# Optimization experiments

Measured on AMD Instinct MI355X. Metric: run time of the kernel, lower is better.

The kernel has to match this reference:

```python
import jax, jax.numpy as jnp
import numpy as np

B, N, CT = 64, 256, 3
HID, HEADS = 256, 4
C = HID // HEADS          # per-head channels
E = 8192                  # number of edges
NEG = 0.2                 # GATv2 leaky_relu negative slope
EPS_BN = 1e-5


def setup_inputs() -> dict:
    key = jax.random.key(0)
    ks = jax.random.split(key, 32)
    F_in = N * CT
    s1 = 1.0 / np.sqrt(F_in)
    sh = 1.0 / np.sqrt(HID)
    inp = {
        "x": jax.random.normal(ks[0], (B, N, N, CT), jnp.float32),
        "edge_index": jax.random.randint(ks[1], (2, E), 0, N, dtype=jnp.int32),
        # node_proj: Linear + BatchNorm1d (eval) params
        "W1": jax.random.normal(ks[2], (F_in, HID), jnp.float32) * s1,
        "b1": jnp.zeros((HID,), jnp.float32),
        "g1": jnp.ones((HID,), jnp.float32),
        "be1": jnp.zeros((HID,), jnp.float32),
        "m1": jnp.zeros((HID,), jnp.float32),
        "v1": jnp.ones((HID,), jnp.float32),
        # GATv2 layer 0
        "Wl0": jax.random.normal(ks[3], (HID, HID), jnp.float32) * sh,
        "bl0": jnp.zeros((HID,), jnp.float32),
        "Wr0": jax.random.normal(ks[4], (HID, HID), jnp.float32) * sh,
        "br0": jnp.zeros((HID,), jnp.float32),
        "att0": jax.random.normal(ks[5], (HEADS, C), jnp.float32) * (1.0 / np.sqrt(C)),
        "bo0": jnp.zeros((HID,), jnp.float32),
        # GATv2 layer 1
        "Wl1": jax.random.normal(ks[6], (HID, HID), jnp.float32) * sh,
        "bl1": jnp.zeros((HID,), jnp.float32),
        "Wr1": jax.random.normal(ks[7], (HID, HID), jnp.float32) * sh,
        "br1": jnp.zeros((HID,), jnp.float32),
        "att1": jax.random.normal(ks[8], (HEADS, C), jnp.float32) * (1.0 / np.sqrt(C)),
        "bo1": jnp.zeros((HID,), jnp.float32),
        # output_proj: Linear + BatchNorm1d (eval) params
        "W2": jax.random.normal(ks[9], (HID, HID), jnp.float32) * sh,
        "b2": jnp.zeros((HID,), jnp.float32),
        "g2": jnp.ones((HID,), jnp.float32),
        "be2": jnp.zeros((HID,), jnp.float32),
        "m2": jnp.zeros((HID,), jnp.float32),
        "v2": jnp.ones((HID,), jnp.float32),
    }
    return inp


def _bn(x, g, b, m, v):
    # BatchNorm1d in eval mode: per-feature affine with running stats
    return (x - m) * jax.lax.rsqrt(v + EPS_BN) * g + b


def _gatv2(h, src, dst, Wl, bl, Wr, br, att, bo):
    # h: (N, HID). GATv2Conv (PyG semantics): lin_l on source, lin_r on target.
    xl = (h @ Wl + bl).reshape(N, HEADS, C)
    xr = (h @ Wr + br).reshape(N, HEADS, C)
    x_j = xl[src]                        # (E, H, C) source features
    x_i = xr[dst]                        # (E, H, C) target features
    e = jax.nn.leaky_relu(x_i + x_j, NEG)
    logits = jnp.einsum('ehc,hc->eh', e, att)          # (E, H)
    mx = jax.ops.segment_max(logits, dst, num_segments=N)
    a = jnp.exp(logits - mx[dst])
    den = jax.ops.segment_sum(a, dst, num_segments=N)
    a = a / (den[dst] + 1e-16)                         # neighborhood softmax
    out = jax.ops.segment_sum(x_j * a[:, :, None], dst, num_segments=N)
    return out.reshape(N, HID) + bo


def reference(x, edge_index, W1, b1, g1, be1, m1, v1,
              Wl0, bl0, Wr0, br0, att0, bo0,
              Wl1, bl1, Wr1, br1, att1, bo1,
              W2, b2, g2, be2, m2, v2):
    gelu = lambda t: jax.nn.gelu(t, approximate=False)
    xf = x.reshape(B, N, N * CT)
    # node_proj (eval: dropout off, BN uses running stats -> vmappable)
    h = gelu(_bn(xf @ W1 + b1, g1, be1, m1, v1))       # (B, N, HID)
    src, dst = edge_index[0], edge_index[1]

    def per_sample(hn):
        h0 = gelu(_gatv2(hn, src, dst, Wl0, bl0, Wr0, br0, att0, bo0))
        h1 = gelu(_gatv2(h0, src, dst, Wl1, bl1, Wr1, br1, att1, bo1))
        return h1.mean(axis=0)                          # mean over nodes

    pooled = jax.vmap(per_sample)(h)                    # (B, HID)
    return gelu(_bn(pooled @ W2 + b2, g2, be2, m2, v2))
```

## Files before the change

### kernel.cpp

```cpp
#include <hip/hip_runtime.h>
#include <hip/hip_bf16.h>
#include <math.h>

#define BATCH   64
#define NNODES  256
#define HID     256
#define HEADS   4
#define CDIM    64
#define NEDGES  8192
#define NEG_SLOPE 0.2f
#define EPS_BN 1e-5f


typedef __bf16 bf16_t;
typedef __bf16 bf16x8 __attribute__((ext_vector_type(8)));
typedef float  f32x4  __attribute__((ext_vector_type(4)));

__device__ __forceinline__ float gelu_f(float x) {
    return 0.5f * x * (1.0f + erff(x * 0.70710678118654752440f));
}

__global__ __launch_bounds__(256) void csr_kernel(const int* __restrict__ ei,
                                                  int* __restrict__ noff,
                                                  int* __restrict__ csrc) {
    __shared__ int cnt[NNODES];
    __shared__ int off_s[NNODES + 1];
    const int tid = threadIdx.x;
    cnt[tid] = 0;
    __syncthreads();
    for (int e = tid; e < NEDGES; e += 256) atomicAdd(&cnt[ei[NEDGES + e]], 1);
    __syncthreads();
    if (tid == 0) {
        int s = 0;
        for (int i = 0; i < NNODES; ++i) { off_s[i] = s; s += cnt[i]; }
        off_s[NNODES] = s;
    }
    __syncthreads();
    cnt[tid] = off_s[tid];
    noff[tid] = off_s[tid];
    if (tid == 0) noff[NNODES] = off_s[NNODES];
    __syncthreads();
    for (int e = tid; e < NEDGES; e += 256) {
        int d = ei[NEDGES + e];
        int p = atomicAdd(&cnt[d], 1);
        csrc[p] = ei[e];
    }
}

__global__ __launch_bounds__(256) void trans_kernel(
        const float* __restrict__ W1, const float* __restrict__ Wa,
        const float* __restrict__ Wb, const float* __restrict__ Wc,
        const float* __restrict__ Wd,
        bf16_t* __restrict__ T1, bf16_t* __restrict__ Ta,
        bf16_t* __restrict__ Tb, bf16_t* __restrict__ Tc,
        bf16_t* __restrict__ Td) {
    __shared__ float tile[32][33];
    int bx = blockIdx.x;
    const float* in; bf16_t* out; int K, t;
    if (bx < 192) { in = W1; out = T1; K = 768; t = bx; }
    else {
        int r = bx - 192, mid = r >> 6; t = r & 63; K = 256;
        if (mid == 0) { in = Wa; out = Ta; }
        else if (mid == 1) { in = Wb; out = Tb; }
        else if (mid == 2) { in = Wc; out = Tc; }
        else { in = Wd; out = Td; }
    }
    const int kt = t >> 3, nt = t & 7;
    const int k0 = kt * 32, n0 = nt * 32;
    const int x = threadIdx.x, y = threadIdx.y;
    #pragma unroll
    for (int j = 0; j < 4; ++j)
        tile[y + j * 8][x] = in[(size_t)(k0 + y + j * 8) * 256 + n0 + x];
    __syncthreads();
    #pragma unroll
    for (int j = 0; j < 4; ++j)
        out[(size_t)(n0 + y + j * 8) * K + k0 + x] = (bf16_t)tile[x][y + j * 8];
}

#define GSTR 56

template<int A_F32, int DUAL, int EPI_BN, int PERM>
__global__ __launch_bounds__(256) void gemm_kernel(
        const void* __restrict__ Ap,
        const bf16_t* __restrict__ Bt0, const bf16_t* __restrict__ Bt1,
        void* __restrict__ C0p, void* __restrict__ C1p, int K,
        const float* __restrict__ bias0, const float* __restrict__ bias1,
        const float* __restrict__ g, const float* __restrict__ be,
        const float* __restrict__ mu, const float* __restrict__ var) {
    __shared__ bf16_t As[128][GSTR];
    __shared__ bf16_t Bs[64][GSTR];
    const int tid  = threadIdx.x;
    const int lane = tid & 63;
    const int wv   = tid >> 6;
    const int wm   = wv >> 1, wn = wv & 1;
    const int mblk = blockIdx.y * 128;
    const int nt   = blockIdx.x;
    const bool second = DUAL && (nt >= 4);
    const bf16_t* Bt = second ? Bt1 : Bt0;
    const int n0 = (second ? (nt - 4) : nt) * 64;

    f32x4 acc[8];
    #pragma unroll
    for (int i = 0; i < 8; ++i) acc[i] = (f32x4){0.f, 0.f, 0.f, 0.f};

    const int arow = tid >> 1, akh = (tid & 1) * 16;
    const int gr   = mblk + arow;
    const int arr  = PERM ? ((gr & 63) * 256 + (gr >> 6)) : gr;
    const int brow = tid >> 2, bkh = (tid & 3) * 8;
    const int fm = lane & 15, kc = (lane >> 4) * 8;

    for (int k0 = 0; k0 < K; k0 += 32) {
        if (A_F32) {
            const float* ap = (const float*)Ap + (size_t)arr * K + k0 + akh;
            f32x4 a0 = *(const f32x4*)ap;
            f32x4 a1 = *(const f32x4*)(ap + 4);
            f32x4 a2 = *(const f32x4*)(ap + 8);
            f32x4 a3 = *(const f32x4*)(ap + 12);
            bf16x8 v0, v1;
            #pragma unroll
            for (int j = 0; j < 4; ++j) {
                v0[j] = (bf16_t)a0[j]; v0[4 + j] = (bf16_t)a1[j];
                v1[j] = (bf16_t)a2[j]; v1[4 + j] = (bf16_t)a3[j];
            }
            *(bf16x8*)(&As[arow][akh])     = v0;
            *(bf16x8*)(&As[arow][akh + 8]) = v1;
        } else {
            const bf16_t* ap = (const bf16_t*)Ap + (size_t)arr * K + k0 + akh;
            *(bf16x8*)(&As[arow][akh])     = *(const bf16x8*)ap;
            *(bf16x8*)(&As[arow][akh + 8]) = *(const bf16x8*)(ap + 8);
        }
        *(bf16x8*)(&Bs[brow][bkh]) =
            *(const bf16x8*)(Bt + (size_t)(n0 + brow) * K + k0 + bkh);
        __syncthreads();

        bf16x8 af[4], bf[2];
        #pragma unroll
        for (int f = 0; f < 4; ++f)
            af[f] = *(const bf16x8*)(&As[wm * 64 + f * 16 + fm][kc]);
        #pragma unroll
        for (int t = 0; t < 2; ++t)
            bf[t] = *(const bf16x8*)(&Bs[wn * 32 + t * 16 + fm][kc]);
        #pragma unroll
        for (int f = 0; f < 4; ++f)
            #pragma unroll
            for (int t = 0; t < 2; ++t)
                acc[f * 2 + t] = __builtin_amdgcn_mfma_f32_16x16x32_bf16(
                    af[f], bf[t], acc[f * 2 + t], 0, 0, 0);
        __syncthreads();
    }

    const int quad = lane >> 4, cn = lane & 15;
    #pragma unroll
    for (int t = 0; t < 2; ++t) {
        const int n = n0 + wn * 32 + t * 16 + cn;
        const float bv = second ? bias1[n] : bias0[n];
        float scale = 1.0f, shift = 0.0f;
        if (EPI_BN) {
            float s = g[n] * rsqrtf(var[n] + EPS_BN);
            scale = s;
            shift = be[n] - mu[n] * s;
        }
        #pragma unroll
        for (int f = 0; f < 4; ++f) {
            #pragma unroll
            for (int r = 0; r < 4; ++r) {
                const int m = mblk + wm * 64 + f * 16 + quad * 4 + r;
                float val = acc[f * 2 + t][r] + bv;
                if (EPI_BN) val = gelu_f(val * scale + shift);
                if (second) ((float*)C1p)[(size_t)m * 256 + n] = val;
                else        ((bf16_t*)C0p)[(size_t)m * 256 + n] = (bf16_t)val;
            }
        }
    }
}

template<int OUT_F32>
__global__ __launch_bounds__(256) void edge_kernel(
        const bf16_t* __restrict__ XL, const float* __restrict__ XR,
        const float* __restrict__ att, const float* __restrict__ bo,
        const int* __restrict__ noff, const int* __restrict__ csrc,
        void* __restrict__ Hout) {
    const int i    = blockIdx.x;
    const int tid  = threadIdx.x;
    const int w    = tid >> 6;
    const int lane = tid & 63;
    const int bg   = lane >> 3;
    const int cg   = lane & 7;
    const int b    = blockIdx.y * 8 + bg;
    const int cbase = w * CDIM + cg * 8;
    const size_t orow = ((size_t)i * BATCH + b) * HID + cbase;

    float a6[8], a4[8], xi[8];
    {
        const float* ar = att + cbase;
        const float* xr = XR + orow;
        #pragma unroll
        for (int q = 0; q < 8; ++q) {
            float a = ar[q];
            a6[q] = 0.6f * a; a4[q] = 0.4f * a;
            xi[q] = xr[q];
        }
    }
    const int s0 = noff[i], s1 = noff[i + 1];

    float m = -1e30f, den = 0.f;
    float acc[8];
    #pragma unroll
    for (int q = 0; q < 8; ++q) acc[q] = 0.f;

    const bf16_t* XLb = XL + (size_t)b * HID + cbase;

    int jc = csrc[s0 < s1 ? s0 : 0];
    bf16x8 xjp = *(const bf16x8*)(XLb + (size_t)jc * (BATCH * HID));

    for (int e = s0; e < s1; ++e) {
        const int en = e + 1;
        const int jn = csrc[en < s1 ? en : s0];
        const bf16x8 xjn = *(const bf16x8*)(XLb + (size_t)jn * (BATCH * HID));

        float xjf[8];
        #pragma unroll
        for (int q = 0; q < 8; ++q) xjf[q] = (float)xjp[q];
        float p = 0.f;
        #pragma unroll
        for (int q = 0; q < 8; ++q) {
            const float z = xi[q] + xjf[q];
            p = fmaf(a6[q], z, p);
            p = fmaf(a4[q], __builtin_fabsf(z), p);
        }
        p += __shfl_xor(p, 1, 64);
        p += __shfl_xor(p, 2, 64);
        p += __shfl_xor(p, 4, 64);

        const float mn = fmaxf(m, p);
        const float alpha = __expf(m - mn);
        const float we = __expf(p - mn);
        den = den * alpha + we;
        #pragma unroll
        for (int q = 0; q < 8; ++q) acc[q] = fmaf(acc[q], alpha, we * xjf[q]);
        m = mn;
        xjp = xjn;
    }

    const float inv = 1.0f / (den + 1e-16f);
    const float* bor = bo + cbase;
    if (OUT_F32) {
        float* op = (float*)Hout + orow;
        #pragma unroll
        for (int q = 0; q < 8; ++q)
            op[q] = gelu_f(acc[q] * inv + bor[q]);
    } else {
        bf16x8 ov;
        #pragma unroll
        for (int q = 0; q < 8; ++q)
            ov[q] = (bf16_t)gelu_f(acc[q] * inv + bor[q]);
        *(bf16x8*)((bf16_t*)Hout + orow) = ov;
    }
}

__global__ __launch_bounds__(256) void pool_kernel(const float* __restrict__ H1,
                                                   float* __restrict__ P) {
    const int b = blockIdx.x, c = blockIdx.y, f = threadIdx.x;
    float s = 0.f;
    for (int n = 0; n < 64; ++n)
        s += H1[((size_t)(c * 64 + n) * BATCH + b) * HID + f];
    P[((size_t)b * 4 + c) * HID + f] = s;
}

__global__ __launch_bounds__(256) void final_kernel(
        const float* __restrict__ P, const float* __restrict__ W2,
        const float* __restrict__ b2, const float* __restrict__ g2,
        const float* __restrict__ be2, const float* __restrict__ m2,
        const float* __restrict__ v2, float* __restrict__ out) {
    __shared__ float pl[HID];
    const int b = blockIdx.x, f = threadIdx.x;
    float s4 = 0.f;
    #pragma unroll
    for (int c = 0; c < 4; ++c) s4 += P[((size_t)b * 4 + c) * HID + f];
    pl[f] = s4 * (1.0f / (float)NNODES);
    __syncthreads();
    float s = 0.f;
    for (int k = 0; k < HID; ++k) s += pl[k] * W2[(size_t)k * HID + f];
    s += b2[f];
    const float scale = g2[f] * rsqrtf(v2[f] + EPS_BN);
    s = (s - m2[f]) * scale + be2[f];
    out[b * HID + f] = gelu_f(s);
}

extern "C" void kernel_launch(void* const* d_in, const int* in_sizes, int n_in,
                              void* d_out, int out_size, void* d_ws, size_t ws_size,
                              hipStream_t stream) {
    const float* x    = (const float*)d_in[0];
    const int*   ei   = (const int*)d_in[1];
    const float* W1   = (const float*)d_in[2];
    const float* b1   = (const float*)d_in[3];
    const float* g1   = (const float*)d_in[4];
    const float* be1  = (const float*)d_in[5];
    const float* m1   = (const float*)d_in[6];
    const float* v1   = (const float*)d_in[7];
    const float* Wl0  = (const float*)d_in[8];
    const float* bl0  = (const float*)d_in[9];
    const float* Wr0  = (const float*)d_in[10];
    const float* br0  = (const float*)d_in[11];
    const float* att0 = (const float*)d_in[12];
    const float* bo0  = (const float*)d_in[13];
    const float* Wl1  = (const float*)d_in[14];
    const float* bl1  = (const float*)d_in[15];
    const float* Wr1  = (const float*)d_in[16];
    const float* br1  = (const float*)d_in[17];
    const float* att1 = (const float*)d_in[18];
    const float* bo1  = (const float*)d_in[19];
    const float* W2   = (const float*)d_in[20];
    const float* b2   = (const float*)d_in[21];
    const float* g2   = (const float*)d_in[22];
    const float* be2  = (const float*)d_in[23];
    const float* m2   = (const float*)d_in[24];
    const float* v2   = (const float*)d_in[25];

    char* ws = (char*)d_ws;
    const int M = BATCH * NNODES;
    const size_t SZ_BF = (size_t)M * HID * sizeof(bf16_t);
    const size_t SZ_F  = (size_t)M * HID * sizeof(float);

    int*    noff = (int*)ws;                ws += 2048;
    int*    csrc = (int*)ws;                ws += 32768;
    bf16_t* W1t  = (bf16_t*)ws;             ws += 256 * 768 * 2;
    bf16_t* Wl0t = (bf16_t*)ws;             ws += 256 * 256 * 2;
    bf16_t* Wr0t = (bf16_t*)ws;             ws += 256 * 256 * 2;
    bf16_t* Wl1t = (bf16_t*)ws;             ws += 256 * 256 * 2;
    bf16_t* Wr1t = (bf16_t*)ws;             ws += 256 * 256 * 2;
    bf16_t* H    = (bf16_t*)ws;             ws += SZ_BF;
    bf16_t* H2   = (bf16_t*)ws;             ws += SZ_BF;
    bf16_t* XL   = (bf16_t*)ws;             ws += SZ_BF;
    float*  XR   = (float*)ws;              ws += SZ_F;
    float*  H1f  = (float*)ws;              ws += SZ_F;
    float*  P    = (float*)ws;              ws += BATCH * 4 * HID * 4;

    csr_kernel<<<1, 256, 0, stream>>>(ei, noff, csrc);
    trans_kernel<<<448, dim3(32, 8), 0, stream>>>(W1, Wl0, Wr0, Wl1, Wr1,
                                                  W1t, Wl0t, Wr0t, Wl1t, Wr1t);

    gemm_kernel<1, 0, 1, 1><<<dim3(4, 128), 256, 0, stream>>>(
        x, W1t, nullptr, H, nullptr, 768, b1, nullptr, g1, be1, m1, v1);

    gemm_kernel<0, 1, 0, 0><<<dim3(8, 128), 256, 0, stream>>>(
        H, Wl0t, Wr0t, XL, XR, 256, bl0, br0, nullptr, nullptr, nullptr, nullptr);
    edge_kernel<0><<<dim3(NNODES, 8), 256, 0, stream>>>(
        XL, XR, att0, bo0, noff, csrc, H2);

    gemm_kernel<0, 1, 0, 0><<<dim3(8, 128), 256, 0, stream>>>(
        H2, Wl1t, Wr1t, XL, XR, 256, bl1, br1, nullptr, nullptr, nullptr, nullptr);
    edge_kernel<1><<<dim3(NNODES, 8), 256, 0, stream>>>(
        XL, XR, att1, bo1, noff, csrc, H1f);

    pool_kernel<<<dim3(BATCH, 4), 256, 0, stream>>>(H1f, P);
    final_kernel<<<BATCH, 256, 0, stream>>>(P, W2, b2, g2, be2, m2, v2,
                                            (float*)d_out);
}
```

Measured before the change: 318.4 us.

## Merge prep kernels, store XR and layer outputs in bf16, dual-chain edge softmax

Merges the CSR build and weight transposes into one launch, and stores the right-projection XR and the final GAT output in bf16 instead of fp32 to cut memory traffic. The edge kernel now runs two independent online-softmax chains over alternating edges for more ILP, merges them at the end, and short-circuits nodes with no incoming edges. The pool and final kernels are fused into one kernel that reads bf16 H directly. The trade-offs are reduced precision in XR and the final activations, and a serial 256-node loop per thread in the fused pool kernel.

```diff
diff --git a/kernel.cpp b/kernel.cpp
--- a/kernel.cpp
+++ b/kernel.cpp
@@ -20,42 +20,42 @@
     return 0.5f * x * (1.0f + erff(x * 0.70710678118654752440f));
 }
 
-__global__ __launch_bounds__(256) void csr_kernel(const int* __restrict__ ei,
-                                                  int* __restrict__ noff,
-                                                  int* __restrict__ csrc) {
-    __shared__ int cnt[NNODES];
-    __shared__ int off_s[NNODES + 1];
-    const int tid = threadIdx.x;
-    cnt[tid] = 0;
-    __syncthreads();
-    for (int e = tid; e < NEDGES; e += 256) atomicAdd(&cnt[ei[NEDGES + e]], 1);
-    __syncthreads();
-    if (tid == 0) {
-        int s = 0;
-        for (int i = 0; i < NNODES; ++i) { off_s[i] = s; s += cnt[i]; }
-        off_s[NNODES] = s;
-    }
-    __syncthreads();
-    cnt[tid] = off_s[tid];
-    noff[tid] = off_s[tid];
-    if (tid == 0) noff[NNODES] = off_s[NNODES];
-    __syncthreads();
-    for (int e = tid; e < NEDGES; e += 256) {
-        int d = ei[NEDGES + e];
-        int p = atomicAdd(&cnt[d], 1);
-        csrc[p] = ei[e];
-    }
-}
-
-__global__ __launch_bounds__(256) void trans_kernel(
+__global__ __launch_bounds__(256) void prep_kernel(
+        const int* __restrict__ ei,
         const float* __restrict__ W1, const float* __restrict__ Wa,
         const float* __restrict__ Wb, const float* __restrict__ Wc,
         const float* __restrict__ Wd,
+        int* __restrict__ noff, int* __restrict__ csrc,
         bf16_t* __restrict__ T1, bf16_t* __restrict__ Ta,
         bf16_t* __restrict__ Tb, bf16_t* __restrict__ Tc,
         bf16_t* __restrict__ Td) {
+    const int bx = blockIdx.x;
+    const int tid = threadIdx.x;
+    if (bx == 448) {
+        __shared__ int cnt[NNODES];
+        __shared__ int off_s[NNODES + 1];
+        cnt[tid] = 0;
+        __syncthreads();
+        for (int e = tid; e < NEDGES; e += 256) atomicAdd(&cnt[ei[NEDGES + e]], 1);
+        __syncthreads();
+        if (tid == 0) {
+            int s = 0;
+            for (int i = 0; i < NNODES; ++i) { off_s[i] = s; s += cnt[i]; }
+            off_s[NNODES] = s;
+        }
+        __syncthreads();
+        cnt[tid] = off_s[tid];
+        noff[tid] = off_s[tid];
+        if (tid == 0) noff[NNODES] = off_s[NNODES];
+        __syncthreads();
+        for (int e = tid; e < NEDGES; e += 256) {
+            int d = ei[NEDGES + e];
+            int p = atomicAdd(&cnt[d], 1);
+            csrc[p] = ei[e];
+        }
+        return;
+    }
     __shared__ float tile[32][33];
-    int bx = blockIdx.x;
     const float* in; bf16_t* out; int K, t;
     if (bx < 192) { in = W1; out = T1; K = 768; t = bx; }
     else {
@@ -67,7 +67,7 @@
     }
     const int kt = t >> 3, nt = t & 7;
     const int k0 = kt * 32, n0 = nt * 32;
-    const int x = threadIdx.x, y = threadIdx.y;
+    const int x = tid & 31, y = tid >> 5;
     #pragma unroll
     for (int j = 0; j < 4; ++j)
         tile[y + j * 8][x] = in[(size_t)(k0 + y + j * 8) * 256 + n0 + x];
@@ -83,7 +83,7 @@
 __global__ __launch_bounds__(256) void gemm_kernel(
         const void* __restrict__ Ap,
         const bf16_t* __restrict__ Bt0, const bf16_t* __restrict__ Bt1,
-        void* __restrict__ C0p, void* __restrict__ C1p, int K,
+        bf16_t* __restrict__ C0p, bf16_t* __restrict__ C1p, int K,
         const float* __restrict__ bias0, const float* __restrict__ bias1,
         const float* __restrict__ g, const float* __restrict__ be,
         const float* __restrict__ mu, const float* __restrict__ var) {
@@ -97,6 +97,7 @@
     const int nt   = blockIdx.x;
     const bool second = DUAL && (nt >= 4);
     const bf16_t* Bt = second ? Bt1 : Bt0;
+    bf16_t* Cp = second ? C1p : C0p;
     const int n0 = (second ? (nt - 4) : nt) * 64;
 
     f32x4 acc[8];
@@ -167,124 +168,136 @@
                 const int m = mblk + wm * 64 + f * 16 + quad * 4 + r;
                 float val = acc[f * 2 + t][r] + bv;
                 if (EPI_BN) val = gelu_f(val * scale + shift);
-                if (second) ((float*)C1p)[(size_t)m * 256 + n] = val;
-                else        ((bf16_t*)C0p)[(size_t)m * 256 + n] = (bf16_t)val;
+                Cp[(size_t)m * 256 + n] = (bf16_t)val;
             }
         }
     }
 }
 
-template<int OUT_F32>
 __global__ __launch_bounds__(256) void edge_kernel(
-        const bf16_t* __restrict__ XL, const float* __restrict__ XR,
+        const bf16_t* __restrict__ XL, const bf16_t* __restrict__ XR,
         const float* __restrict__ att, const float* __restrict__ bo,
         const int* __restrict__ noff, const int* __restrict__ csrc,
-        void* __restrict__ Hout) {
-    const int i    = blockIdx.x;
+        bf16_t* __restrict__ Hout) {
+    const int bid  = blockIdx.x;
+    const int i    = bid >> 3;
     const int tid  = threadIdx.x;
     const int w    = tid >> 6;
     const int lane = tid & 63;
     const int bg   = lane >> 3;
     const int cg   = lane & 7;
-    const int b    = blockIdx.y * 8 + bg;
+    const int b    = (bid & 7) * 8 + bg;
     const int cbase = w * CDIM + cg * 8;
     const size_t orow = ((size_t)i * BATCH + b) * HID + cbase;
+    const float* bor = bo + cbase;
+
+    const int s0 = noff[i], s1 = noff[i + 1];
+    if (s0 == s1) {
+        bf16x8 ov;
+        #pragma unroll
+        for (int q = 0; q < 8; ++q) ov[q] = (bf16_t)gelu_f(bor[q]);
+        *(bf16x8*)(Hout + orow) = ov;
+        return;
+    }
 
     float a6[8], a4[8], xi[8];
     {
         const float* ar = att + cbase;
-        const float* xr = XR + orow;
+        const bf16x8 xr = *(const bf16x8*)(XR + orow);
         #pragma unroll
         for (int q = 0; q < 8; ++q) {
             float a = ar[q];
             a6[q] = 0.6f * a; a4[q] = 0.4f * a;
-            xi[q] = xr[q];
-        }
-    }
-    const int s0 = noff[i], s1 = noff[i + 1];
-
-    float m = -1e30f, den = 0.f;
-    float acc[8];
-    #pragma unroll
-    for (int q = 0; q < 8; ++q) acc[q] = 0.f;
+            xi[q] = (float)xr[q];
+        }
+    }
 
     const bf16_t* XLb = XL + (size_t)b * HID + cbase;
-
-    int jc = csrc[s0 < s1 ? s0 : 0];
-    bf16x8 xjp = *(const bf16x8*)(XLb + (size_t)jc * (BATCH * HID));
-
-    for (int e = s0; e < s1; ++e) {
-        const int en = e + 1;
-        const int jn = csrc[en < s1 ? en : s0];
-        const bf16x8 xjn = *(const bf16x8*)(XLb + (size_t)jn * (BATCH * HID));
-
-        float xjf[8];
-        #pragma unroll
-        for (int q = 0; q < 8; ++q) xjf[q] = (float)xjp[q];
-        float p = 0.f;
+    const size_t RSTR = (size_t)BATCH * HID;
+
+    float mA = -1e30f, dA = 0.f, mB = -1e30f, dB = 0.f;
+    float accA[8], accB[8];
+    #pragma unroll
+    for (int q = 0; q < 8; ++q) { accA[q] = 0.f; accB[q] = 0.f; }
+
+    int jA = csrc[s0];
+    int jB = csrc[(s0 + 1 < s1) ? s0 + 1 : s0];
+    bf16x8 xA = *(const bf16x8*)(XLb + (size_t)jA * RSTR);
+    bf16x8 xB = *(const bf16x8*)(XLb + (size_t)jB * RSTR);
+
+    for (int e = s0; e < s1; e += 2) {
+        const int nA = (e + 2 < s1) ? e + 2 : s0;
+        const int nB = (e + 3 < s1) ? e + 3 : s0;
+        const int jnA = csrc[nA], jnB = csrc[nB];
+        const bf16x8 xnA = *(const bf16x8*)(XLb + (size_t)jnA * RSTR);
+        const bf16x8 xnB = *(const bf16x8*)(XLb + (size_t)jnB * RSTR);
+
+        float fA[8], fB[8];
+        #pragma unroll
+        for (int q = 0; q < 8; ++q) { fA[q] = (float)xA[q]; fB[q] = (float)xB[q]; }
+        float pA = 0.f, pB = 0.f;
         #pragma unroll
         for (int q = 0; q < 8; ++q) {
-            const float z = xi[q] + xjf[q];
-            p = fmaf(a6[q], z, p);
-            p = fmaf(a4[q], __builtin_fabsf(z), p);
-        }
-        p += __shfl_xor(p, 1, 64);
-        p += __shfl_xor(p, 2, 64);
-        p += __shfl_xor(p, 4, 64);
-
-        const float mn = fmaxf(m, p);
-        const float alpha = __expf(m - mn);
-        const float we = __expf(p - mn);
-        den = den * alpha + we;
-        #pragma unroll
-        for (int q = 0; q < 8; ++q) acc[q] = fmaf(acc[q], alpha, we * xjf[q]);
-        m = mn;
-        xjp = xjn;
-    }
-
-    const float inv = 1.0f / (den + 1e-16f);
-    const float* bor = bo + cbase;
-    if (OUT_F32) {
-        float* op = (float*)Hout + orow;
-        #pragma unroll
-        for (int q = 0; q < 8; ++q)
-            op[q] = gelu_f(acc[q] * inv + bor[q]);
-    } else {
-        bf16x8 ov;
-        #pragma unroll
-        for (int q = 0; q < 8; ++q)
-            ov[q] = (bf16_t)gelu_f(acc[q] * inv + bor[q]);
-        *(bf16x8*)((bf16_t*)Hout + orow) = ov;
-    }
-}
-
-__global__ __launch_bounds__(256) void pool_kernel(const float* __restrict__ H1,
-                                                   float* __restrict__ P) {
-    const int b = blockIdx.x, c = blockIdx.y, f = threadIdx.x;
-    float s = 0.f;
-    for (int n = 0; n < 64; ++n)
-        s += H1[((size_t)(c * 64 + n) * BATCH + b) * HID + f];
-    P[((size_t)b * 4 + c) * HID + f] = s;
-}
-
-__global__ __launch_bounds__(256) void final_kernel(
-        const float* __restrict__ P, const float* __restrict__ W2,
+            const float zA = xi[q] + fA[q];
+            const float zB = xi[q] + fB[q];
+            pA = fmaf(a6[q], zA, pA);
+            pB = fmaf(a6[q], zB, pB);
+            pA = fmaf(a4[q], __builtin_fabsf(zA), pA);
+            pB = fmaf(a4[q], __builtin_fabsf(zB), pB);
+        }
+        pA += __shfl_xor(pA, 1, 64);  pB += __shfl_xor(pB, 1, 64);
+        pA += __shfl_xor(pA, 2, 64);  pB += __shfl_xor(pB, 2, 64);
+        pA += __shfl_xor(pA, 4, 64);  pB += __shfl_xor(pB, 4, 64);
+
+        const float mnA = fmaxf(mA, pA);
+        const float alA = __expf(mA - mnA);
+        const float wA  = __expf(pA - mnA);
+        const float vB  = (e + 1 < s1) ? 1.f : 0.f;
+        const float mnB = fmaxf(mB, pB);
+        const float alB = __expf(mB - mnB);
+        const float wB  = __expf(pB - mnB) * vB;
+        dA = dA * alA + wA;
+        dB = dB * alB + wB;
+        #pragma unroll
+        for (int q = 0; q < 8; ++q) {
+            accA[q] = fmaf(accA[q], alA, wA * fA[q]);
+            accB[q] = fmaf(accB[q], alB, wB * fB[q]);
+        }
+        mA = mnA; mB = mnB;
+        xA = xnA; xB = xnB;
+    }
+
+    const float mm = fmaxf(mA, mB);
+    const float g1 = __expf(mA - mm);
+    const float g2 = __expf(mB - mm);
+    const float inv = 1.0f / (dA * g1 + dB * g2 + 1e-16f);
+    bf16x8 ov;
+    #pragma unroll
+    for (int q = 0; q < 8; ++q) {
+        const float o = (accA[q] * g1 + accB[q] * g2) * inv + bor[q];
+        ov[q] = (bf16_t)gelu_f(o);
+    }
+    *(bf16x8*)(Hout + orow) = ov;
+}
+
+__global__ __launch_bounds__(256) void pf_kernel(
+        const bf16_t* __restrict__ H1, const float* __restrict__ W2,
         const float* __restrict__ b2, const float* __restrict__ g2,
         const float* __restrict__ be2, const float* __restrict__ m2,
         const float* __restrict__ v2, float* __restrict__ out) {
     __shared__ float pl[HID];
     const int b = blockIdx.x, f = threadIdx.x;
-    float s4 = 0.f;
-    #pragma unroll
-    for (int c = 0; c < 4; ++c) s4 += P[((size_t)b * 4 + c) * HID + f];
-    pl[f] = s4 * (1.0f / (float)NNODES);
+    float s = 0.f;
+    for (int n = 0; n < NNODES; ++n)
+        s += (float)H1[((size_t)n * BATCH + b) * HID + f];
+    pl[f] = s * (1.0f / (float)NNODES);
     __syncthreads();
-    float s = 0.f;
-    for (int k = 0; k < HID; ++k) s += pl[k] * W2[(size_t)k * HID + f];
-    s += b2[f];
+    float acc = 0.f;
+    for (int k = 0; k < HID; ++k) acc += pl[k] * W2[(size_t)k * HID + f];
+    acc += b2[f];
     const float scale = g2[f] * rsqrtf(v2[f] + EPS_BN);
-    s = (s - m2[f]) * scale + be2[f];
-    out[b * HID + f] = gelu_f(s);
+    acc = (acc - m2[f]) * scale + be2[f];
+    out[b * HID + f] = gelu_f(acc);
 }
 
 extern "C" void kernel_launch(void* const* d_in, const int* in_sizes, int n_in,
@@ -320,7 +333,6 @@
     char* ws = (char*)d_ws;
     const int M = BATCH * NNODES;
     const size_t SZ_BF = (size_t)M * HID * sizeof(bf16_t);
-    const size_t SZ_F  = (size_t)M * HID * sizeof(float);
 
     int*    noff = (int*)ws;                ws += 2048;
     int*    csrc = (int*)ws;                ws += 32768;
@@ -332,28 +344,21 @@
     bf16_t* H    = (bf16_t*)ws;             ws += SZ_BF;
     bf16_t* H2   = (bf16_t*)ws;             ws += SZ_BF;
     bf16_t* XL   = (bf16_t*)ws;             ws += SZ_BF;
-    float*  XR   = (float*)ws;              ws += SZ_F;
-    float*  H1f  = (float*)ws;              ws += SZ_F;
-    float*  P    = (float*)ws;              ws += BATCH * 4 * HID * 4;
-
-    csr_kernel<<<1, 256, 0, stream>>>(ei, noff, csrc);
-    trans_kernel<<<448, dim3(32, 8), 0, stream>>>(W1, Wl0, Wr0, Wl1, Wr1,
-                                                  W1t, Wl0t, Wr0t, Wl1t, Wr1t);
+    bf16_t* XR   = (bf16_t*)ws;             ws += SZ_BF;
+
+    prep_kernel<<<449, 256, 0, stream>>>(ei, W1, Wl0, Wr0, Wl1, Wr1,
+                                         noff, csrc, W1t, Wl0t, Wr0t, Wl1t, Wr1t);
 
     gemm_kernel<1, 0, 1, 1><<<dim3(4, 128), 256, 0, stream>>>(
         x, W1t, nullptr, H, nullptr, 768, b1, nullptr, g1, be1, m1, v1);
 
     gemm_kernel<0, 1, 0, 0><<<dim3(8, 128), 256, 0, stream>>>(
         H, Wl0t, Wr0t, XL, XR, 256, bl0, br0, nullptr, nullptr, nullptr, nullptr);
-    edge_kernel<0><<<dim3(NNODES, 8), 256, 0, stream>>>(
-        XL, XR, att0, bo0, noff, csrc, H2);
+    edge_kernel<<<NNODES * 8, 256, 0, stream>>>(XL, XR, att0, bo0, noff, csrc, H2);
 
     gemm_kernel<0, 1, 0, 0><<<dim3(8, 128), 256, 0, stream>>>(
         H2, Wl1t, Wr1t, XL, XR, 256, bl1, br1, nullptr, nullptr, nullptr, nullptr);
-    edge_kernel<1><<<dim3(NNODES, 8), 256, 0, stream>>>(
-        XL, XR, att1, bo1, noff, csrc, H1f);
-
-    pool_kernel<<<dim3(BATCH, 4), 256, 0, stream>>>(H1f, P);
-    final_kernel<<<BATCH, 256, 0, stream>>>(P, W2, b2, g2, be2, m2, v2,
-                                            (float*)d_out);
-}
+    edge_kernel<<<NNODES * 8, 256, 0, stream>>>(XL, XR, att1, bo1, noff, csrc, H);
+
+    pf_kernel<<<BATCH, 256, 0, stream>>>(H, W2, b2, g2, be2, m2, v2, (float*)d_out);
+}
```

Result: faster. 305.1 us (-4.2%).
